# Kernel optimization log

Measured on AMD Instinct MI355X. Metric: run time of the kernel, lower is better.

Reference implementation:

```python
import jax, jax.numpy as jnp
import numpy as np

AMBIENT = [2, 2, 2]
DEGREES = [a + 1 for a in AMBIENT]          # coords per projective factor
N_COORDS = sum(DEGREES)                      # 9
STARTS = np.concatenate([[0], np.cumsum(DEGREES)[:-1]])
CONST_MULT = 1.0
CLIP = 1.0e6


def _get_real_imag_of_prod(cp):
    """cp: complex [B, n]. Returns (real [B, n(n+1)/2], imag [B, n(n-1)/2]).
    Matches TF boolean_mask(transpose(...)) ordering: row-major (b, a) with b<=a;
    real = (XX+YY)[x, b, a] (symmetric), imag = +XY_YX[x, b, a] for b<a."""
    X, Y = jnp.real(cp), jnp.imag(cp)
    XX_YY = jnp.einsum('xa,xb->xab', X, X) + jnp.einsum('xa,xb->xab', Y, Y)
    XY = jnp.einsum('xa,xb->xab', X, Y)
    XY_YX = XY - XY.transpose(0, 2, 1)      # antisymmetric
    n = cp.shape[1]
    iu = jnp.triu_indices(n)                # incl. diagonal
    su = jnp.triu_indices(n, 1)             # strict upper
    real = XX_YY[:, iu[0], iu[1]]
    imag = XY_YX[:, su[0], su[1]]
    return real, imag


def _bihom(points):
    """points: complex [B, N_COORDS] -> real [B, 729] section products / kappa."""
    B = points.shape[0]
    kappas_prod = jnp.ones((B,), points.real.dtype)
    it_r = it_i = None
    for i, (s, d) in enumerate(zip(STARTS, DEGREES)):
        cp = points[:, s:s + d]
        kappas_prod = kappas_prod * jnp.sum(jnp.abs(cp) ** 2, axis=-1)
        r, im = _get_real_imag_of_prod(cp)
        if i == 0:
            it_r, it_i = r, im
        else:
            new_r = jnp.concatenate([
                jnp.einsum('bi,bj->bij', it_r, r).reshape(B, -1),
                -jnp.einsum('bi,bj->bij', it_i, im).reshape(B, -1)], axis=1)
            new_i = jnp.concatenate([
                jnp.einsum('bi,bj->bij', it_r, im).reshape(B, -1),
                -jnp.einsum('bi,bj->bij', it_i, r).reshape(B, -1)], axis=1)
            it_r, it_i = new_r, new_i
    sec = jnp.concatenate([it_r, it_i], axis=-1)
    return sec / kappas_prod[:, None]


def _tower(h, W1, b1, W2, b2, W3, b3, Wf):
    # Dense layers with square activation, then log|.| into bias-free final Dense
    h = (h @ W1 + b1) ** 2
    h = (h @ W2 + b2) ** 2
    h = (h @ W3 + b3) ** 2
    return jnp.log(jnp.abs(h)) @ Wf


def setup_inputs() -> dict:
    key = jax.random.key(0)
    ks = jax.random.split(key, 16)
    B = 32768
    s = 0.05
    inp = {
        'x':   jax.random.normal(ks[0], (B, 2 * N_COORDS), jnp.float32),
        'W1a': jax.random.normal(ks[1], (729, 1024), jnp.float32) * s,
        'b1a': jax.random.normal(ks[2], (1024,), jnp.float32) * s,
        'W2a': jax.random.normal(ks[3], (1024, 1024), jnp.float32) * s,
        'b2a': jax.random.normal(ks[4], (1024,), jnp.float32) * s,
        'W3a': jax.random.normal(ks[5], (1024, 1), jnp.float32) * s,
        'b3a': jax.random.normal(ks[6], (1,), jnp.float32) * s,
        'Wfa': jnp.ones((1, 1), jnp.float32),
        'W1b': jax.random.normal(ks[7], (729, 1024), jnp.float32) * s,
        'b1b': jax.random.normal(ks[8], (1024,), jnp.float32) * s,
        'W2b': jax.random.normal(ks[9], (1024, 1024), jnp.float32) * s,
        'b2b': jax.random.normal(ks[10], (1024,), jnp.float32) * s,
        'W3b': jax.random.normal(ks[11], (1024, 1), jnp.float32) * s,
        'b3b': jax.random.normal(ks[12], (1,), jnp.float32) * s,
        'Wfb': jnp.ones((1, 1), jnp.float32),
    }
    return inp


def reference(x, W1a, b1a, W2a, b2a, W3a, b3a, Wfa,
              W1b, b1b, W2b, b2b, W3b, b3b, Wfb):
    points = jax.lax.complex(x[:, :N_COORDS], x[:, N_COORDS:])
    feats = _bihom(points)                     # [B, 729]
    out = _tower(feats, W1a, b1a, W2a, b2a, W3a, b3a, Wfa) \
        - _tower(feats, W1b, b1b, W2b, b2b, W3b, b3b, Wfb)
    return CONST_MULT * jnp.clip(out, -CLIP, CLIP)
```

## Files before the change

### kernel.cpp

```cpp
#include <hip/hip_runtime.h>

typedef unsigned short u16;
typedef unsigned int u32;
typedef __attribute__((ext_vector_type(8))) short bf16x8;
typedef __attribute__((ext_vector_type(4))) float f32x4;
typedef __attribute__((ext_vector_type(2))) unsigned int u32x2;
typedef __attribute__((ext_vector_type(4))) unsigned int u32x4;

__device__ __forceinline__ u16 f2bf(float x){
  unsigned u = __builtin_bit_cast(unsigned, x);
  unsigned r = (u + 0x7FFFu + ((u >> 16) & 1u)) >> 16;
  return (u16)r;
}
__device__ __forceinline__ float bf2f(u16 h){
  unsigned u = ((unsigned)h) << 16;
  return __builtin_bit_cast(float, u);
}

__device__ __forceinline__ void gld_lds16(const void* g, void* l){
  __builtin_amdgcn_global_load_lds((const __attribute__((address_space(1))) void*)g,
                                   (__attribute__((address_space(3))) void*)l,
                                   16, 0, 0);
}

__global__ void wconv_kernel(const float* __restrict__ W0, u16* __restrict__ Th0, int K0p,
                             const float* __restrict__ W1, u16* __restrict__ Th1, int K1p,
                             const float* __restrict__ W2, u16* __restrict__ Th2, int K2p,
                             const float* __restrict__ W3, u16* __restrict__ Th3, int K3p)
{
  __shared__ float t[32][33];
  int z = blockIdx.z;
  const float* W = z==0 ? W0 : z==1 ? W1 : z==2 ? W2 : W3;
  u16* Th = z==0 ? Th0 : z==1 ? Th1 : z==2 ? Th2 : Th3;
  int Kpad = z==0 ? K0p : z==1 ? K1p : z==2 ? K2p : K3p;
  int K = (Kpad == 768) ? 729 : 1024;
  int k0 = blockIdx.x * 32;
  if (k0 >= Kpad) return;
  int n0 = blockIdx.y * 32;
  int tx = threadIdx.x & 31, ty = threadIdx.x >> 5;
#pragma unroll
  for (int j = 0; j < 4; j++){
    int k = k0 + ty + j*8;
    float v = (k < K) ? W[(size_t)k*1024 + (n0 + tx)] : 0.f;
    t[ty + j*8][tx] = v;
  }
  __syncthreads();
#pragma unroll
  for (int j = 0; j < 4; j++){
    int n = n0 + ty + j*8;
    int k = k0 + tx;
    size_t idx = (size_t)n*Kpad + k;
    Th[idx] = f2bf(t[tx][ty + j*8]);
  }
}

__global__ void feats_kernel(const float* __restrict__ x,
                             u16* __restrict__ fh,
                             int row0)
{
  __shared__ float cC[8][28];
  __shared__ float tA[8][81];
  __shared__ float tB[8][12];
  __shared__ float ivk[8];
  const int tid = threadIdx.x;
  const int lrow0 = blockIdx.x * 8;
  if (tid < 8){
    const float* xr = x + (size_t)(row0 + lrow0 + tid) * 18;
    float kk = 1.f;
#pragma unroll
    for (int f = 0; f < 3; f++){
      float xa = xr[3*f+0], xb = xr[3*f+1], xc = xr[3*f+2];
      float ya = xr[9+3*f+0], yb = xr[9+3*f+1], yc = xr[9+3*f+2];
      int bse = f * 9;
      cC[tid][bse+0] = xa*xa + ya*ya;
      cC[tid][bse+1] = xa*xb + ya*yb;
      cC[tid][bse+2] = xa*xc + ya*yc;
      cC[tid][bse+3] = xb*xb + yb*yb;
      cC[tid][bse+4] = xb*xc + yb*yc;
      cC[tid][bse+5] = xc*xc + yc*yc;
      cC[tid][bse+6] = xa*yb - xb*ya;
      cC[tid][bse+7] = xa*yc - xc*ya;
      cC[tid][bse+8] = xb*yc - xc*yb;
      kk *= (xa*xa+ya*ya + xb*xb+yb*yb + xc*xc+yc*yc);
    }
    ivk[tid] = 1.f / kk;
#pragma unroll
    for (int j = 0; j < 6; j++) tB[tid][j] = cC[tid][18+j];
#pragma unroll
    for (int j = 0; j < 3; j++) tB[tid][6+j] = cC[tid][24+j];
  }
  __syncthreads();
#pragma unroll 1
  for (int e = tid; e < 648; e += 256){
    int r = e / 81;
    int k = e - r*81;
    const float* cc = cC[r];
    float val;
    if (k < 36)      {               val =   cc[k/6]     * cc[9  + k%6]; }
    else if (k < 45) { int u = k-36; val = -(cc[6 + u/3] * cc[15 + u%3]); }
    else if (k < 63) { int u = k-45; val =   cc[u/3]     * cc[15 + u%3]; }
    else             { int u = k-63; val = -(cc[6 + u/6] * cc[9  + u%6]); }
    tA[r][k] = val;
  }
  __syncthreads();
#pragma unroll 1
  for (int jj = 0; jj < 3; jj++){
    int o = jj*256 + tid;
    int idxA = 0, idxB = 0; float sgn = 0.f;
    if (o < 270)      {              idxA = o/6;      idxB = o - (o/6)*6; sgn =  1.f; }
    else if (o < 378) { int t = o-270; idxA = 45 + t/3; idxB = 6 + t%3;   sgn = -1.f; }
    else if (o < 513) { int t = o-378; idxA = t/3;      idxB = 6 + t%3;   sgn =  1.f; }
    else if (o < 729) { int t = o-513; idxA = 45 + t/6; idxB = t%6;       sgn = -1.f; }
#pragma unroll
    for (int r = 0; r < 8; r++){
      float v = sgn * tA[r][idxA] * tB[r][idxB] * ivk[r];
      size_t oi = (size_t)(lrow0 + r) * 768 + o;
      fh[oi] = f2bf(v);
    }
  }
}

#define GEMM_SMEM_BYTES (49152*2 + 4096)

#define STAGE(BUF) do{ \
    u16* _a = sA + (BUF)*8192; u16* _b = sB + (BUF)*8192; \
    gld_lds16(gAh0, _a + wave*1024); gld_lds16(gAh1, _a + wave*1024 + 512); \
    gld_lds16(gBh0, _b + wave*1024); gld_lds16(gBh1, _b + wave*1024 + 512); \
    gAh0 += 32; gAh1 += 32; gBh0 += 32; gBh1 += 32; \
  }while(0)

#define BARRIER()  asm volatile("s_barrier" ::: "memory")
#define LGKM0()    asm volatile("s_waitcnt lgkmcnt(0)" ::: "memory")

template<int MODE>
__global__ __launch_bounds__(512, 1) void gemm_k(
    const u16* __restrict__ Aa, const u16* __restrict__ Ab,
    const u16* __restrict__ Ba, const u16* __restrict__ Bb,
    const float* __restrict__ biasa, const float* __restrict__ biasb,
    u16* __restrict__ Oa, u16* __restrict__ Ob,
    const float* __restrict__ W3a_, const float* __restrict__ W3b_,
    float* __restrict__ Pa, float* __restrict__ Pb, int Pstride,
    int K)
{
  extern __shared__ __align__(16) u16 smem[];
  u16* sA = smem;
  u16* sB = smem + 24576;
  float* rowsum = (float*)(smem + 49152);

  const int nwg = gridDim.x;
  const int qq = nwg >> 3;
  const int wg = (nwg & 7) ? (int)blockIdx.x
                           : ((blockIdx.x & 7) * qq + (blockIdx.x >> 3));
  const int nb = wg & 3;
  const int tower = (wg >> 2) & 1;
  const int mb = wg >> 3;

  const u16* Ahi = tower ? Ab : Aa;
  const u16* Bhi = tower ? Bb : Ba;
  const float* bias = tower ? biasb : biasa;

  const int tid = threadIdx.x;
  const int wave = tid >> 6, lane = tid & 63;
  const int wm = wave >> 2, wn = wave & 3;

  const int l4 = lane >> 2, ls = lane & 3;
  const int fsw  = (l4 >> 1) & 3;
  const int koff = ((ls ^ fsw) << 3);

  const u16* gAh0 = Ahi + (size_t)(mb*256 + wave*32 + l4) * K + koff;
  const u16* gAh1 = gAh0 + (size_t)16 * K;
  const u16* gBh0 = Bhi + (size_t)(nb*256 + wave*32 + l4) * K + koff;
  const u16* gBh1 = gBh0 + (size_t)16 * K;

  const int r16 = lane & 15, g = lane >> 4;
  const int fr   = (r16 >> 1) & 3;
  const int slot = ((g ^ fr) << 3);

  f32x4 acc[8][4];
#pragma unroll
  for (int m = 0; m < 8; m++)
#pragma unroll
    for (int n = 0; n < 4; n++)
      acc[m][n] = (f32x4){0.f, 0.f, 0.f, 0.f};

  const int NT = K >> 5;
  STAGE(0); STAGE(1);

#pragma unroll 1
  for (int t = 0; t < NT; ++t){
    if (t + 1 < NT){
      asm volatile("s_waitcnt vmcnt(4)" ::: "memory");
    } else {
      asm volatile("s_waitcnt vmcnt(0)" ::: "memory");
    }
    BARRIER();
    if (t + 2 < NT){
      int b2 = (t + 2) % 3;
      STAGE(b2);
    }
    const int cur = t % 3;
    const u16* pA = sA + cur*8192;
    const u16* pB = sB + cur*8192;
    bf16x8 ah[8], bh[4];
#pragma unroll
    for (int n = 0; n < 4; n++) bh[n] = *(const bf16x8*)(pB + (wn*64 + n*16 + r16)*32 + slot);
#pragma unroll
    for (int m = 0; m < 8; m++) ah[m] = *(const bf16x8*)(pA + (wm*128 + m*16 + r16)*32 + slot);
    __builtin_amdgcn_s_setprio(1);
#pragma unroll
    for (int m = 0; m < 8; m++)
#pragma unroll
      for (int n = 0; n < 4; n++)
        acc[m][n] = __builtin_amdgcn_mfma_f32_16x16x32_bf16(ah[m], bh[n], acc[m][n], 0, 0, 0);
    __builtin_amdgcn_s_setprio(0);
  }

  if constexpr (MODE == 0){
    u16* Oh = tower ? Ob : Oa;
    float bv[4];
#pragma unroll
    for (int n = 0; n < 4; n++) bv[n] = bias[nb*256 + wn*64 + n*16 + r16];
    __syncthreads();
    u16* wbuf = smem + wave*1088;
    const int rr = lane >> 2, c4 = lane & 3;
#pragma unroll
    for (int m = 0; m < 8; m++){
#pragma unroll
      for (int n = 0; n < 4; n++)
#pragma unroll
        for (int q = 0; q < 4; q++){
          float val = acc[m][n][q] + bv[n];
          val = val * val;
          wbuf[(g*4 + q)*68 + n*16 + r16] = f2bf(val);
        }
      LGKM0();
      const u16* rp = wbuf + rr*68 + c4*16;
      u32x2 d0 = *(const u32x2*)(rp);
      u32x2 d1 = *(const u32x2*)(rp + 4);
      u32x2 d2 = *(const u32x2*)(rp + 8);
      u32x2 d3 = *(const u32x2*)(rp + 12);
      size_t grow = (size_t)(mb*256 + wm*128 + m*16 + rr);
      u16* gp = Oh + grow*1024 + nb*256 + wn*64 + c4*16;
      u32x4 s0 = (u32x4){d0[0], d0[1], d1[0], d1[1]};
      u32x4 s1 = (u32x4){d2[0], d2[1], d3[0], d3[1]};
      *(u32x4*)(gp)     = s0;
      *(u32x4*)(gp + 8) = s1;
      LGKM0();
    }
  } else {
    const float* W3 = tower ? W3b_ : W3a_;
    float* P = tower ? Pb : Pa;
    float w3v[4], bv[4];
#pragma unroll
    for (int n = 0; n < 4; n++){
      int col = nb*256 + wn*64 + n*16 + r16;
      w3v[n] = W3[col];
      bv[n]  = bias[col];
    }
    float rp[8][4];
#pragma unroll
    for (int m = 0; m < 8; m++)
#pragma unroll
      for (int q = 0; q < 4; q++)
        rp[m][q] = 0.f;
#pragma unroll
    for (int m = 0; m < 8; m++)
#pragma unroll
      for (int n = 0; n < 4; n++)
#pragma unroll
        for (int q = 0; q < 4; q++){
          float v = acc[m][n][q] + bv[n];
          rp[m][q] += v * v * w3v[n];
        }
#pragma unroll
    for (int m = 0; m < 8; m++)
#pragma unroll
      for (int q = 0; q < 4; q++){
        float s = rp[m][q];
        s += __shfl_xor(s, 1); s += __shfl_xor(s, 2);
        s += __shfl_xor(s, 4); s += __shfl_xor(s, 8);
        rp[m][q] = s;
      }
    if (r16 == 0){
#pragma unroll
      for (int m = 0; m < 8; m++)
#pragma unroll
        for (int q = 0; q < 4; q++)
          rowsum[wn*256 + wm*128 + m*16 + g*4 + q] = rp[m][q];
    }
    __syncthreads();
    if (tid < 256){
      float s = rowsum[tid] + rowsum[256 + tid] + rowsum[512 + tid] + rowsum[768 + tid];
      P[(size_t)nb * Pstride + mb*256 + tid] = s;
    }
  }
}

__global__ void finalize_kernel(const float* __restrict__ Pa, const float* __restrict__ Pb,
                                int Pstride,
                                const float* __restrict__ b3a, const float* __restrict__ Wfa,
                                const float* __restrict__ b3b, const float* __restrict__ Wfb,
                                float* __restrict__ out, int row0, int Rc)
{
  int r = blockIdx.x * 256 + threadIdx.x;
  if (r >= Rc) return;
  float sa = b3a[0], sb = b3b[0];
#pragma unroll
  for (int j = 0; j < 4; j++){
    sa += Pa[(size_t)j * Pstride + r];
    sb += Pb[(size_t)j * Pstride + r];
  }
  float ta = 2.f * logf(fabsf(sa)) * Wfa[0];
  float tb = 2.f * logf(fabsf(sb)) * Wfb[0];
  float o = ta - tb;
  o = fminf(fmaxf(o, -1000000.f), 1000000.f);
  out[row0 + r] = o;
}

static inline size_t align256(size_t v){ return (v + 255) & ~(size_t)255; }

extern "C" void kernel_launch(void* const* d_in, const int* in_sizes, int n_in,
                              void* d_out, int out_size, void* d_ws, size_t ws_size,
                              hipStream_t stream)
{
  (void)n_in; (void)out_size;
  const float* x   = (const float*)d_in[0];
  const float* W1a = (const float*)d_in[1];
  const float* b1a = (const float*)d_in[2];
  const float* W2a = (const float*)d_in[3];
  const float* b2a = (const float*)d_in[4];
  const float* W3a = (const float*)d_in[5];
  const float* b3a = (const float*)d_in[6];
  const float* Wfa = (const float*)d_in[7];
  const float* W1b = (const float*)d_in[8];
  const float* b1b = (const float*)d_in[9];
  const float* W2b = (const float*)d_in[10];
  const float* b2b = (const float*)d_in[11];
  const float* W3b = (const float*)d_in[12];
  const float* b3b = (const float*)d_in[13];
  const float* Wfb = (const float*)d_in[14];
  float* out = (float*)d_out;

  const int B  = in_sizes[0] / 18;
  const int K1 = 768;
  const int K2 = 1024;

  hipFuncSetAttribute((const void*)gemm_k<0>,
                      hipFuncAttributeMaxDynamicSharedMemorySize, GEMM_SMEM_BYTES);
  hipFuncSetAttribute((const void*)gemm_k<1>,
                      hipFuncAttributeMaxDynamicSharedMemorySize, GEMM_SMEM_BYTES);

  char* base = (char*)d_ws;
  size_t off = 0;
  auto carve = [&](size_t bytes) -> char* {
    off = align256(off);
    char* p = base + off;
    off += bytes;
    return p;
  };

  u16* wt1a = (u16*)carve((size_t)1024 * K1 * 2);
  u16* wt2a = (u16*)carve((size_t)1024 * K2 * 2);
  u16* wt1b = (u16*)carve((size_t)1024 * K1 * 2);
  u16* wt2b = (u16*)carve((size_t)1024 * K2 * 2);

  size_t fixed = align256(off);
  const long long per_row = (long long)K1*2 + 4096 + 64;
  long long avail = (long long)ws_size - (long long)fixed - 8192;
  long long rmax = avail > 0 ? avail / per_row : 0;
  int R = (int)((rmax / 256) * 256);
  if (R > B) R = B;
  if (R < 256) R = 256;

  u16* fh   = (u16*)carve((size_t)R * K1 * 2);
  u16* h1a  = (u16*)carve((size_t)R * 1024 * 2);
  u16* h1b  = (u16*)carve((size_t)R * 1024 * 2);
  float* pa = (float*)carve((size_t)4 * R * 4);
  float* pb = (float*)carve((size_t)4 * R * 4);

  wconv_kernel<<<dim3(32, 32, 4), 256, 0, stream>>>(
      W1a, wt1a, K1,
      W2a, wt2a, K2,
      W1b, wt1b, K1,
      W2b, wt2b, K2);

  for (int row0 = 0; row0 < B; row0 += R){
    int Rc = B - row0; if (Rc > R) Rc = R;
    int MB = Rc / 256;
    feats_kernel<<<Rc/8, 256, 0, stream>>>(x, fh, row0);
    gemm_k<0><<<dim3(8*MB), 512, GEMM_SMEM_BYTES, stream>>>(
        fh, fh, wt1a, wt1b, b1a, b1b,
        h1a, h1b, nullptr, nullptr, nullptr, nullptr, 0, K1);
    gemm_k<1><<<dim3(8*MB), 512, GEMM_SMEM_BYTES, stream>>>(
        h1a, h1b, wt2a, wt2b, b2a, b2b,
        nullptr, nullptr, W3a, W3b, pa, pb, R, K2);
    finalize_kernel<<<(Rc + 255)/256, 256, 0, stream>>>(pa, pb, R, b3a, Wfa, b3b, Wfb,
                                                        out, row0, Rc);
  }
}
```

Before: 268.1 us.

## Pre-pack weights into MFMA fragment layout and load B directly to registers

```diff
diff --git a/kernel.cpp b/kernel.cpp
--- a/kernel.cpp
+++ b/kernel.cpp
@@ -45,13 +45,21 @@
     t[ty + j*8][tx] = v;
   }
   __syncthreads();
-#pragma unroll
-  for (int j = 0; j < 4; j++){
-    int n = n0 + ty + j*8;
-    int k = k0 + tx;
-    size_t idx = (size_t)n*Kpad + k;
-    Th[idx] = f2bf(t[tx][ty + j*8]);
-  }
+  const int NKB = Kpad >> 5;
+  const int kblk = k0 >> 5;
+  int flat = threadIdx.x * 4;
+  int f    = flat >> 9;
+  int idx  = flat & 511;
+  int g    = idx >> 7;
+  int rr   = (idx >> 3) & 15;
+  int j0   = idx & 7;
+  u16 v0 = f2bf(t[g*8 + j0 + 0][f*16 + rr]);
+  u16 v1 = f2bf(t[g*8 + j0 + 1][f*16 + rr]);
+  u16 v2 = f2bf(t[g*8 + j0 + 2][f*16 + rr]);
+  u16 v3 = f2bf(t[g*8 + j0 + 3][f*16 + rr]);
+  size_t base = ((size_t)((n0 >> 4) + f) * NKB + kblk) * 512 + idx;
+  u32x2 pk = (u32x2){ (u32)v0 | ((u32)v1 << 16), (u32)v2 | ((u32)v3 << 16) };
+  *(u32x2*)(Th + base) = pk;
 }
 
 __global__ void feats_kernel(const float* __restrict__ x,
@@ -120,17 +128,41 @@
   }
 }
 
-#define GEMM_SMEM_BYTES (49152*2 + 4096)
-
-#define STAGE(BUF) do{ \
-    u16* _a = sA + (BUF)*8192; u16* _b = sB + (BUF)*8192; \
+#define GEMM_SMEM_BYTES (49152 + 4096)
+
+#define STAGE_A(BUF) do{ \
+    u16* _a = sA + (BUF)*8192; \
     gld_lds16(gAh0, _a + wave*1024); gld_lds16(gAh1, _a + wave*1024 + 512); \
-    gld_lds16(gBh0, _b + wave*1024); gld_lds16(gBh1, _b + wave*1024 + 512); \
-    gAh0 += 32; gAh1 += 32; gBh0 += 32; gBh1 += 32; \
+    gAh0 += 32; gAh1 += 32; \
   }while(0)
 
 #define BARRIER()  asm volatile("s_barrier" ::: "memory")
 #define LGKM0()    asm volatile("s_waitcnt lgkmcnt(0)" ::: "memory")
+#define VM2()      asm volatile("s_waitcnt vmcnt(2)" ::: "memory")
+
+#define SUBSTEP(T, BUSE, BLOAD, LDGUARD, STGUARD) do{ \
+    VM2(); \
+    BARRIER(); \
+    if (LDGUARD){ \
+      _Pragma("unroll") \
+      for (int n_ = 0; n_ < 4; n_++) \
+        BLOAD[n_] = *(const bf16x8*)(gB + ((size_t)n_*NKB + (T)+1)*512); \
+    } \
+    if (STGUARD){ STAGE_A(((T)+2)%3); } \
+    { \
+      const u16* pA = sA + ((T)%3)*8192; \
+      bf16x8 ah[8]; \
+      _Pragma("unroll") \
+      for (int m_ = 0; m_ < 8; m_++) ah[m_] = *(const bf16x8*)(pA + (wm*128 + m_*16 + r16)*32 + slot); \
+      __builtin_amdgcn_s_setprio(1); \
+      _Pragma("unroll") \
+      for (int m_ = 0; m_ < 8; m_++) \
+        _Pragma("unroll") \
+        for (int n_ = 0; n_ < 4; n_++) \
+          acc[m_][n_] = __builtin_amdgcn_mfma_f32_16x16x32_bf16(ah[m_], BUSE[n_], acc[m_][n_], 0, 0, 0); \
+      __builtin_amdgcn_s_setprio(0); \
+    } \
+  }while(0)
 
 template<int MODE>
 __global__ __launch_bounds__(512, 1) void gemm_k(
@@ -144,8 +176,7 @@
 {
   extern __shared__ __align__(16) u16 smem[];
   u16* sA = smem;
-  u16* sB = smem + 24576;
-  float* rowsum = (float*)(smem + 49152);
+  float* rowsum = (float*)(smem + 24576);
 
   const int nwg = gridDim.x;
   const int qq = nwg >> 3;
@@ -156,12 +187,13 @@
   const int mb = wg >> 3;
 
   const u16* Ahi = tower ? Ab : Aa;
-  const u16* Bhi = tower ? Bb : Ba;
+  const u16* Bf  = tower ? Bb : Ba;
   const float* bias = tower ? biasb : biasa;
 
   const int tid = threadIdx.x;
   const int wave = tid >> 6, lane = tid & 63;
   const int wm = wave >> 2, wn = wave & 3;
+  const int NKB = K >> 5;
 
   const int l4 = lane >> 2, ls = lane & 3;
   const int fsw  = (l4 >> 1) & 3;
@@ -169,8 +201,8 @@
 
   const u16* gAh0 = Ahi + (size_t)(mb*256 + wave*32 + l4) * K + koff;
   const u16* gAh1 = gAh0 + (size_t)16 * K;
-  const u16* gBh0 = Bhi + (size_t)(nb*256 + wave*32 + l4) * K + koff;
-  const u16* gBh1 = gBh0 + (size_t)16 * K;
+
+  const u16* gB = Bf + ((size_t)(nb*16 + wn*4) * NKB) * 512 + lane*8;
 
   const int r16 = lane & 15, g = lane >> 4;
   const int fr   = (r16 >> 1) & 3;
@@ -184,35 +216,15 @@
       acc[m][n] = (f32x4){0.f, 0.f, 0.f, 0.f};
 
   const int NT = K >> 5;
-  STAGE(0); STAGE(1);
+  STAGE_A(0); STAGE_A(1);
+  bf16x8 b0[4], b1[4];
+#pragma unroll
+  for (int n = 0; n < 4; n++) b0[n] = *(const bf16x8*)(gB + ((size_t)n*NKB)*512);
 
 #pragma unroll 1
-  for (int t = 0; t < NT; ++t){
-    if (t + 1 < NT){
-      asm volatile("s_waitcnt vmcnt(4)" ::: "memory");
-    } else {
-      asm volatile("s_waitcnt vmcnt(0)" ::: "memory");
-    }
-    BARRIER();
-    if (t + 2 < NT){
-      int b2 = (t + 2) % 3;
-      STAGE(b2);
-    }
-    const int cur = t % 3;
-    const u16* pA = sA + cur*8192;
-    const u16* pB = sB + cur*8192;
-    bf16x8 ah[8], bh[4];
-#pragma unroll
-    for (int n = 0; n < 4; n++) bh[n] = *(const bf16x8*)(pB + (wn*64 + n*16 + r16)*32 + slot);
-#pragma unroll
-    for (int m = 0; m < 8; m++) ah[m] = *(const bf16x8*)(pA + (wm*128 + m*16 + r16)*32 + slot);
-    __builtin_amdgcn_s_setprio(1);
-#pragma unroll
-    for (int m = 0; m < 8; m++)
-#pragma unroll
-      for (int n = 0; n < 4; n++)
-        acc[m][n] = __builtin_amdgcn_mfma_f32_16x16x32_bf16(ah[m], bh[n], acc[m][n], 0, 0, 0);
-    __builtin_amdgcn_s_setprio(0);
+  for (int t = 0; t < NT; t += 2){
+    SUBSTEP(t,   b0, b1, true,        (t+2 < NT));
+    SUBSTEP(t+1, b1, b0, (t+2 < NT),  (t+3 < NT));
   }
 
   if constexpr (MODE == 0){
@@ -220,6 +232,7 @@
     float bv[4];
 #pragma unroll
     for (int n = 0; n < 4; n++) bv[n] = bias[nb*256 + wn*64 + n*16 + r16];
+    asm volatile("s_waitcnt vmcnt(0)" ::: "memory");
     __syncthreads();
     u16* wbuf = smem + wave*1088;
     const int rr = lane >> 2, c4 = lane & 3;
```

New measurement: 276.3 us. 3.1% more time.
